# Performance work log

Measured on AMD Instinct MI355X. Metric: run time of the kernel, lower is better.

## Reference

```python
import jax, jax.numpy as jnp
import numpy as np

TOKENS, IN_F, OUT_F = 8192, 4096, 4096
MAXQ = 15          # 4-bit
ZERO_POINT = 8     # (maxq + 1) // 2


def _make_24_mask(key, in_f, out_f):
    """Boolean 2:4 mask: exactly 2 True per contiguous group of 4 along in_f."""
    scores = jax.random.normal(key, (in_f // 4, 4, out_f), dtype=jnp.float32)
    # ascending sort along the group-of-4 axis; index 2 = 2nd largest value
    thresh = jnp.sort(scores, axis=1)[:, 2:3, :]
    mask = scores >= thresh  # keeps top-2 of each group of 4
    return mask.reshape(in_f, out_f)


def setup_inputs() -> dict:
    key = jax.random.key(0)
    k_x, k_q, k_m, k_s = jax.random.split(key, 4)
    x = jax.random.normal(k_x, (TOKENS, IN_F), dtype=jnp.float16)
    qvals = jax.random.randint(k_q, (IN_F, OUT_F), 0, MAXQ + 1, dtype=jnp.int32)
    mask = _make_24_mask(k_m, IN_F, OUT_F)
    # per-column scales (groupsize == infeatures -> one scale row)
    scales = (jax.random.uniform(k_s, (1, OUT_F), dtype=jnp.float32) * 0.01 + 0.001).astype(jnp.float16)
    return {"x": x, "qvals": qvals, "mask": mask, "scales": scales}


def reference(x, qvals, mask, scales):
    # Dequantize: W = (q - zero_point) * scale, then apply 2:4 sparsity mask.
    w = (qvals.astype(jnp.float32) - ZERO_POINT) * scales.astype(jnp.float32)  # [in, out]
    w = jnp.where(mask, w, 0.0).astype(x.dtype)
    # GEMM with fp32 accumulation (as the fused kernel does), output in x.dtype
    y = jnp.einsum("ti,io->to", x, w, preferred_element_type=jnp.float32)
    return y.astype(x.dtype)
```

## Files before the change

kernel.cpp:

```cpp
#include <hip/hip_runtime.h>
#include <stdint.h>

typedef short short8 __attribute__((ext_vector_type(8)));
typedef float floatx4 __attribute__((ext_vector_type(4)));

#define M_TOK 8192
#define K_IN  4096
#define N_OUT 4096
#define NTT   (K_IN / 32)

static __device__ __forceinline__ float bf2f(ushort u) {
    union { uint32_t u; float f; } v;
    v.u = ((uint32_t)u) << 16;
    return v.f;
}
static __device__ __forceinline__ ushort f2bf(float f) {
    union { float f; uint32_t u; } v;
    v.f = f;
    uint32_t u = v.u;
    uint32_t r = (u + 0x7FFFu + ((u >> 16) & 1u)) >> 16;
    return (ushort)r;
}

__global__ void detect_zero_kernel(int* __restrict__ flags) {
    if (threadIdx.x < 3) flags[1 + threadIdx.x] = 0;
}

__global__ __launch_bounds__(256) void detect_count_kernel(
    const unsigned char* __restrict__ mb, int* __restrict__ flags) {
    const ushort* mh = (const ushort*)mb;
    const unsigned int* mw = (const unsigned int*)mb;
    __shared__ int sh[3];
    if (threadIdx.x < 3) sh[threadIdx.x] = 0;
    __syncthreads();
    int s = blockIdx.x * 256 + threadIdx.x;
    int grp = s & 255;
    int o   = (s * 97) & 4095;
    int c1 = 0, c2 = 0, c4 = 0;
    #pragma unroll
    for (int r = 0; r < 4; ++r) {
        size_t idx = (size_t)(4 * grp + r) * N_OUT + o;
        c1 += (mb[idx] != 0);
        c2 += (mh[idx] != 0);
        c4 += (mw[idx] != 0);
    }
    if (c1 != 2) atomicAdd(&sh[0], 1);
    if (c2 != 2) atomicAdd(&sh[1], 1);
    if (c4 != 2) atomicAdd(&sh[2], 1);
    __syncthreads();
    if (threadIdx.x == 0) {
        atomicAdd(&flags[1], sh[0]);
        atomicAdd(&flags[2], sh[1]);
        atomicAdd(&flags[3], sh[2]);
    }
}

__global__ void detect_final_kernel(int* __restrict__ flags) {
    if (threadIdx.x == 0) {
        int size = 4, best = flags[3];
        if (flags[2] < best) { size = 2; best = flags[2]; }
        if (flags[1] < best) { size = 1; }
        flags[0] = size;
    }
}

__global__ __launch_bounds__(256) void convert_x_kernel(
    const float* __restrict__ xf, ushort* __restrict__ Xb) {
    const int total = M_TOK * K_IN;
    const int stride = gridDim.x * 256 * 8;
    for (int i = (blockIdx.x * 256 + threadIdx.x) * 8; i < total; i += stride) {
        floatx4 f0 = *(const floatx4*)&xf[i];
        floatx4 f1 = *(const floatx4*)&xf[i + 4];
        short8 v;
        #pragma unroll
        for (int j = 0; j < 4; ++j) v[j]     = (short)f2bf(f0[j]);
        #pragma unroll
        for (int j = 0; j < 4; ++j) v[4 + j] = (short)f2bf(f1[j]);
        *(short8*)&Xb[i] = v;
    }
}

__global__ __launch_bounds__(256) void dequant_kernel(
    const int* __restrict__ q, const void* __restrict__ maskp,
    const float* __restrict__ scales, ushort* __restrict__ Bt,
    const int* __restrict__ flagp) {
    const int msize = flagp[0];
    const int i0 = blockIdx.x * 64;
    const int o0 = blockIdx.y * 64;
    const int tid = threadIdx.x;
    const unsigned char* mb = (const unsigned char*)maskp;
    const ushort* mh = (const ushort*)maskp;
    const unsigned int* mi = (const unsigned int*)maskp;
    __shared__ ushort T[64][72];

    for (int p = 0; p < 16; ++p) {
        int idx = p * 256 + tid;
        int r = idx >> 6, c = idx & 63;
        size_t gi = (size_t)(i0 + r) * N_OUT + (o0 + c);
        bool m;
        if (msize == 1)      m = (mb[gi] != 0);
        else if (msize == 2) m = (mh[gi] != 0);
        else                 m = (mi[gi] != 0);
        float s = scales[o0 + c];
        float w = m ? (float)(q[gi] - 8) * s : 0.0f;
        T[r][c] = f2bf(w);
    }
    __syncthreads();
    for (int p = 0; p < 2; ++p) {
        int ol = p * 32 + (tid >> 3);
        int i8 = (tid & 7) * 8;
        short8 v;
        #pragma unroll
        for (int j = 0; j < 8; ++j) v[j] = (short)T[i8 + j][ol];
        *(short8*)&Bt[(size_t)(o0 + ol) * K_IN + i0 + i8] = v;
    }
}

#define GL2L16(gp, lbase)                                                      \
    __builtin_amdgcn_global_load_lds(                                          \
        (const __attribute__((address_space(1))) void*)(gp),                   \
        (__attribute__((address_space(3))) void*)(lbase), 16, 0, 0)

#define MFMA16(a, b, c) __builtin_amdgcn_mfma_f32_16x16x32_bf16(a, b, c, 0, 0, 0)

__global__ __launch_bounds__(256, 2) void gemm_kernel(
    const ushort* __restrict__ X,
    const ushort* __restrict__ Bt,
    float* __restrict__ Y) {
    __shared__ ushort As[2][128][32];
    __shared__ ushort Bs[2][256][32];

    const int tid  = threadIdx.x;
    const int w    = tid >> 6;
    const int lane = tid & 63;

    const int xcd = blockIdx.x & 7;
    const int jj  = (blockIdx.x >> 3) & 63;
    const int rr0 = blockIdx.x >> 9;
    const int m_tile = rr0 * 32 + (xcd & 1) * 16 + (jj & 15);
    const int n_tile = (xcd >> 1) * 4 + (jj >> 4);
    const int row0 = m_tile * 128;
    const int col0 = n_tile * 256;

    floatx4 acc[8][4] = {};

    const int schunk = (tid & 3) ^ ((tid >> 3) & 3);
    const ushort* gA = X  + (size_t)(row0 + (tid >> 2)) * K_IN + schunk * 8;
    const ushort* gB = Bt + (size_t)(col0 + (tid >> 2)) * K_IN + schunk * 8;

    const int fr = lane & 15, g = lane >> 4;
    const int fsw = (fr >> 1) & 3;

    #define STG(BF, tt)                                                        \
        do {                                                                   \
            GL2L16(gA + (size_t)(tt) * 32,                                     \
                   (char*)&As[BF][w * 16][0] + lane * 16);                     \
            GL2L16(gA + (size_t)64 * K_IN + (size_t)(tt) * 32,                 \
                   (char*)&As[BF][64 + w * 16][0] + lane * 16);                \
            GL2L16(gB + (size_t)(tt) * 32,                                     \
                   (char*)&Bs[BF][w * 16][0] + lane * 16);                     \
            GL2L16(gB + (size_t)64 * K_IN + (size_t)(tt) * 32,                 \
                   (char*)&Bs[BF][64 + w * 16][0] + lane * 16);                \
            GL2L16(gB + (size_t)128 * K_IN + (size_t)(tt) * 32,                \
                   (char*)&Bs[BF][128 + w * 16][0] + lane * 16);               \
            GL2L16(gB + (size_t)192 * K_IN + (size_t)(tt) * 32,                \
                   (char*)&Bs[BF][192 + w * 16][0] + lane * 16);               \
        } while (0)

    #define TILE(BF, T)                                                        \
        do {                                                                   \
            short8 afr[8], bfr[4];                                             \
            _Pragma("unroll")                                                  \
            for (int n = 0; n < 4; ++n)                                        \
                bfr[n] = *(const short8*)&Bs[BF][w * 64 + n * 16 + fr]         \
                             [(g ^ fsw) * 8];                                  \
            _Pragma("unroll")                                                  \
            for (int m = 0; m < 8; ++m)                                        \
                afr[m] = *(const short8*)&As[BF][m * 16 + fr][(g ^ fsw) * 8];  \
            if ((T) + 1 < NTT) STG((BF) ^ 1, (T) + 1);                         \
            __builtin_amdgcn_s_barrier();                                      \
            asm volatile("s_waitcnt lgkmcnt(0)" ::: "memory");                 \
            __builtin_amdgcn_sched_barrier(0);                                 \
            __builtin_amdgcn_s_setprio(1);                                     \
            _Pragma("unroll")                                                  \
            for (int m = 0; m < 8; ++m)                                        \
                _Pragma("unroll")                                              \
                for (int n = 0; n < 4; ++n)                                    \
                    acc[m][n] = MFMA16(afr[m], bfr[n], acc[m][n]);             \
            __builtin_amdgcn_s_setprio(0);                                     \
            asm volatile("s_waitcnt vmcnt(0)" ::: "memory");                   \
            __builtin_amdgcn_s_barrier();                                      \
        } while (0)

    STG(0, 0);
    asm volatile("s_waitcnt vmcnt(0)" ::: "memory");
    __builtin_amdgcn_s_barrier();

    for (int t = 0; t < NTT; t += 2) {
        TILE(0, t);
        TILE(1, t + 1);
    }

    const int fq = lane >> 4;
    #pragma unroll
    for (int m = 0; m < 8; ++m)
        #pragma unroll
        for (int n = 0; n < 4; ++n)
            #pragma unroll
            for (int i = 0; i < 4; ++i) {
                int rr = row0 + m * 16 + fq * 4 + i;
                int cc = col0 + w * 64 + n * 16 + fr;
                Y[(size_t)rr * N_OUT + cc] = acc[m][n][i];
            }
    #undef TILE
    #undef STG
}

__global__ __launch_bounds__(256) void fallback_kernel(
    const float* __restrict__ xf, const int* __restrict__ q,
    const void* __restrict__ maskp, const float* __restrict__ scales,
    float* __restrict__ Y, const int* __restrict__ flagp) {
    const int msize = flagp[0];
    const int o = blockIdx.x * 256 + threadIdx.x;
    const int t = blockIdx.y;
    const unsigned char* mb = (const unsigned char*)maskp;
    const ushort* mh = (const ushort*)maskp;
    const unsigned int* mi = (const unsigned int*)maskp;
    float s = scales[o];
    float acc = 0.f;
    for (int i = 0; i < K_IN; ++i) {
        float x = bf2f(f2bf(xf[(size_t)t * K_IN + i]));
        size_t gi = (size_t)i * N_OUT + o;
        bool m;
        if (msize == 1)      m = (mb[gi] != 0);
        else if (msize == 2) m = (mh[gi] != 0);
        else                 m = (mi[gi] != 0);
        if (m) acc += x * bf2f(f2bf((float)(q[gi] - 8) * s));
    }
    Y[(size_t)t * N_OUT + o] = acc;
}

extern "C" void kernel_launch(void* const* d_in, const int* in_sizes, int n_in,
                              void* d_out, int out_size, void* d_ws, size_t ws_size,
                              hipStream_t stream) {
    const float* x      = (const float*)d_in[0];
    const int*   q      = (const int*)d_in[1];
    const void*  mask   = d_in[2];
    const float* scales = (const float*)d_in[3];
    float* y = (float*)d_out;

    const size_t BT_OFF = 64;
    const size_t XB_OFF = BT_OFF + (size_t)N_OUT * K_IN * 2;
    const size_t need   = XB_OFF + (size_t)M_TOK * K_IN * 2;

    int* flags = (int*)d_ws;
    detect_zero_kernel<<<1, 64, 0, stream>>>(flags);
    detect_count_kernel<<<64, 256, 0, stream>>>(
        (const unsigned char*)mask, flags);
    detect_final_kernel<<<1, 64, 0, stream>>>(flags);

    if (ws_size >= need) {
        ushort* Bt = (ushort*)((char*)d_ws + BT_OFF);
        ushort* Xb = (ushort*)((char*)d_ws + XB_OFF);
        convert_x_kernel<<<4096, 256, 0, stream>>>(x, Xb);
        dequant_kernel<<<dim3(K_IN / 64, N_OUT / 64), 256, 0, stream>>>(
            q, mask, scales, Bt, flags);
        gemm_kernel<<<dim3((M_TOK / 128) * (N_OUT / 256)), 256, 0, stream>>>(
            Xb, Bt, y);
    } else {
        fallback_kernel<<<dim3(N_OUT / 256, M_TOK), 256, 0, stream>>>(
            x, q, mask, scales, y, flags);
    }
}
```

Baseline: 361.6 us.

## Triple-buffer GEMM LDS pipeline and merge prep kernels into fewer launches

The GEMM now uses three LDS stages and prefetches two K-tiles ahead, waiting only on the older loads (vmcnt(6)) rather than draining all memory traffic each step. The x conversion and weight dequant run as a single prep launch, and the three-kernel mask detection becomes one single-block kernel. The aims are better hiding of global-load latency and less launch overhead. The costs are 50% more LDS per block, which may limit occupancy with two blocks per CU, plus a tail loop unrolled by hand.

After: 360.1 us. No clear change (-0.4%).

```diff
diff --git a/kernel.cpp b/kernel.cpp
--- a/kernel.cpp
+++ b/kernel.cpp
@@ -22,97 +22,84 @@
     return (ushort)r;
 }
 
-__global__ void detect_zero_kernel(int* __restrict__ flags) {
-    if (threadIdx.x < 3) flags[1 + threadIdx.x] = 0;
-}
-
-__global__ __launch_bounds__(256) void detect_count_kernel(
+__global__ __launch_bounds__(256) void detect_kernel(
     const unsigned char* __restrict__ mb, int* __restrict__ flags) {
     const ushort* mh = (const ushort*)mb;
     const unsigned int* mw = (const unsigned int*)mb;
-    __shared__ int sh[3];
-    if (threadIdx.x < 3) sh[threadIdx.x] = 0;
+    __shared__ int v[3];
+    if (threadIdx.x < 3) v[threadIdx.x] = 0;
     __syncthreads();
-    int s = blockIdx.x * 256 + threadIdx.x;
-    int grp = s & 255;
-    int o   = (s * 97) & 4095;
-    int c1 = 0, c2 = 0, c4 = 0;
-    #pragma unroll
-    for (int r = 0; r < 4; ++r) {
-        size_t idx = (size_t)(4 * grp + r) * N_OUT + o;
-        c1 += (mb[idx] != 0);
-        c2 += (mh[idx] != 0);
-        c4 += (mw[idx] != 0);
-    }
-    if (c1 != 2) atomicAdd(&sh[0], 1);
-    if (c2 != 2) atomicAdd(&sh[1], 1);
-    if (c4 != 2) atomicAdd(&sh[2], 1);
+    int l0 = 0, l1 = 0, l2 = 0;
+    for (int o = threadIdx.x; o < 4096; o += 256) {
+        int c1 = 0, c2 = 0, c4 = 0;
+        #pragma unroll
+        for (int r = 0; r < 4; ++r) {
+            int idx = r * N_OUT + o;
+            c1 += (mb[idx] != 0);
+            c2 += (mh[idx] != 0);
+            c4 += (mw[idx] != 0);
+        }
+        l0 += (c1 != 2); l1 += (c2 != 2); l2 += (c4 != 2);
+    }
+    atomicAdd(&v[0], l0); atomicAdd(&v[1], l1); atomicAdd(&v[2], l2);
     __syncthreads();
     if (threadIdx.x == 0) {
-        atomicAdd(&flags[1], sh[0]);
-        atomicAdd(&flags[2], sh[1]);
-        atomicAdd(&flags[3], sh[2]);
-    }
-}
-
-__global__ void detect_final_kernel(int* __restrict__ flags) {
-    if (threadIdx.x == 0) {
-        int size = 4, best = flags[3];
-        if (flags[2] < best) { size = 2; best = flags[2]; }
-        if (flags[1] < best) { size = 1; }
+        int size = 4, best = v[2];
+        if (v[1] < best) { size = 2; best = v[1]; }
+        if (v[0] < best) { size = 1; }
         flags[0] = size;
     }
 }
 
-__global__ __launch_bounds__(256) void convert_x_kernel(
-    const float* __restrict__ xf, ushort* __restrict__ Xb) {
-    const int total = M_TOK * K_IN;
-    const int stride = gridDim.x * 256 * 8;
-    for (int i = (blockIdx.x * 256 + threadIdx.x) * 8; i < total; i += stride) {
-        floatx4 f0 = *(const floatx4*)&xf[i];
-        floatx4 f1 = *(const floatx4*)&xf[i + 4];
-        short8 v;
-        #pragma unroll
-        for (int j = 0; j < 4; ++j) v[j]     = (short)f2bf(f0[j]);
-        #pragma unroll
-        for (int j = 0; j < 4; ++j) v[4 + j] = (short)f2bf(f1[j]);
-        *(short8*)&Xb[i] = v;
-    }
-}
-
-__global__ __launch_bounds__(256) void dequant_kernel(
+__global__ __launch_bounds__(256) void prep_kernel(
+    const float* __restrict__ xf, ushort* __restrict__ Xb,
     const int* __restrict__ q, const void* __restrict__ maskp,
     const float* __restrict__ scales, ushort* __restrict__ Bt,
     const int* __restrict__ flagp) {
-    const int msize = flagp[0];
-    const int i0 = blockIdx.x * 64;
-    const int o0 = blockIdx.y * 64;
     const int tid = threadIdx.x;
-    const unsigned char* mb = (const unsigned char*)maskp;
-    const ushort* mh = (const ushort*)maskp;
-    const unsigned int* mi = (const unsigned int*)maskp;
-    __shared__ ushort T[64][72];
-
-    for (int p = 0; p < 16; ++p) {
-        int idx = p * 256 + tid;
-        int r = idx >> 6, c = idx & 63;
-        size_t gi = (size_t)(i0 + r) * N_OUT + (o0 + c);
-        bool m;
-        if (msize == 1)      m = (mb[gi] != 0);
-        else if (msize == 2) m = (mh[gi] != 0);
-        else                 m = (mi[gi] != 0);
-        float s = scales[o0 + c];
-        float w = m ? (float)(q[gi] - 8) * s : 0.0f;
-        T[r][c] = f2bf(w);
-    }
-    __syncthreads();
-    for (int p = 0; p < 2; ++p) {
-        int ol = p * 32 + (tid >> 3);
-        int i8 = (tid & 7) * 8;
-        short8 v;
-        #pragma unroll
-        for (int j = 0; j < 8; ++j) v[j] = (short)T[i8 + j][ol];
-        *(short8*)&Bt[(size_t)(o0 + ol) * K_IN + i0 + i8] = v;
+    if (blockIdx.x < 4096) {
+        const int total = M_TOK * K_IN;
+        const int stride = 4096 * 256 * 8;
+        for (int i = (blockIdx.x * 256 + tid) * 8; i < total; i += stride) {
+            floatx4 f0 = *(const floatx4*)&xf[i];
+            floatx4 f1 = *(const floatx4*)&xf[i + 4];
+            short8 v;
+            #pragma unroll
+            for (int j = 0; j < 4; ++j) v[j]     = (short)f2bf(f0[j]);
+            #pragma unroll
+            for (int j = 0; j < 4; ++j) v[4 + j] = (short)f2bf(f1[j]);
+            *(short8*)&Xb[i] = v;
+        }
+    } else {
+        const int d  = blockIdx.x - 4096;
+        const int i0 = (d & 63) * 64;
+        const int o0 = (d >> 6) * 64;
+        const int msize = flagp[0];
+        const unsigned char* mb = (const unsigned char*)maskp;
+        const ushort* mh = (const ushort*)maskp;
+        const unsigned int* mi = (const unsigned int*)maskp;
+        __shared__ ushort T[64][72];
+        for (int p = 0; p < 16; ++p) {
+            int idx = p * 256 + tid;
+            int r = idx >> 6, c = idx & 63;
+            size_t gi = (size_t)(i0 + r) * N_OUT + (o0 + c);
+            bool m;
+            if (msize == 1)      m = (mb[gi] != 0);
+            else if (msize == 2) m = (mh[gi] != 0);
+            else                 m = (mi[gi] != 0);
+            float s = scales[o0 + c];
+            float w = m ? (float)(q[gi] - 8) * s : 0.0f;
+            T[r][c] = f2bf(w);
+        }
+        __syncthreads();
+        for (int p = 0; p < 2; ++p) {
+            int ol = p * 32 + (tid >> 3);
+            int i8 = (tid & 7) * 8;
+            short8 v;
+            #pragma unroll
+            for (int j = 0; j < 8; ++j) v[j] = (short)T[i8 + j][ol];
+            *(short8*)&Bt[(size_t)(o0 + ol) * K_IN + i0 + i8] = v;
+        }
     }
 }
 
@@ -127,8 +114,8 @@
     const ushort* __restrict__ X,
     const ushort* __restrict__ Bt,
     float* __restrict__ Y) {
-    __shared__ ushort As[2][128][32];
-    __shared__ ushort Bs[2][256][32];
+    __shared__ ushort As[3][128][32];
+    __shared__ ushort Bs[3][256][32];
 
     const int tid  = threadIdx.x;
     const int w    = tid >> 6;
@@ -151,33 +138,34 @@
     const int fr = lane & 15, g = lane >> 4;
     const int fsw = (fr >> 1) & 3;
 
-    #define STG(BF, tt)                                                        \
+    #define STG(SL, tt)                                                        \
         do {                                                                   \
             GL2L16(gA + (size_t)(tt) * 32,                                     \
-                   (char*)&As[BF][w * 16][0] + lane * 16);                     \
+                   (char*)&As[SL][w * 16][0] + lane * 16);                     \
             GL2L16(gA + (size_t)64 * K_IN + (size_t)(tt) * 32,                 \
-                   (char*)&As[BF][64 + w * 16][0] + lane * 16);                \
+                   (char*)&As[SL][64 + w * 16][0] + lane * 16);                \
             GL2L16(gB + (size_t)(tt) * 32,                                     \
-                   (char*)&Bs[BF][w * 16][0] + lane * 16);                     \
+                   (char*)&Bs[SL][w * 16][0] + lane * 16);                     \
             GL2L16(gB + (size_t)64 * K_IN + (size_t)(tt) * 32,                 \
-                   (char*)&Bs[BF][64 + w * 16][0] + lane * 16);                \
+                   (char*)&Bs[SL][64 + w * 16][0] + lane * 16);                \
             GL2L16(gB + (size_t)128 * K_IN + (size_t)(tt) * 32,                \
-                   (char*)&Bs[BF][128 + w * 16][0] + lane * 16);               \
+                   (char*)&Bs[SL][128 + w * 16][0] + lane * 16);               \
             GL2L16(gB + (size_t)192 * K_IN + (size_t)(tt) * 32,                \
-                   (char*)&Bs[BF][192 + w * 16][0] + lane * 16);               \
+                   (char*)&Bs[SL][192 + w * 16][0] + lane * 16);               \
         } while (0)
 
-    #define TILE(BF, T)                                                        \
+    #define TILE(SL, T)                                                        \
         do {                                                                   \
+            const bool sg = (T) + 2 < NTT;                                     \
             short8 afr[8], bfr[4];                                             \
             _Pragma("unroll")                                                  \
             for (int n = 0; n < 4; ++n)                                        \
-                bfr[n] = *(const short8*)&Bs[BF][w * 64 + n * 16 + fr]         \
+                bfr[n] = *(const short8*)&Bs[SL][w * 64 + n * 16 + fr]         \
                              [(g ^ fsw) * 8];                                  \
             _Pragma("unroll")                                                  \
             for (int m = 0; m < 8; ++m)                                        \
-                afr[m] = *(const short8*)&As[BF][m * 16 + fr][(g ^ fsw) * 8];  \
-            if ((T) + 1 < NTT) STG((BF) ^ 1, (T) + 1);                         \
+                afr[m] = *(const short8*)&As[SL][m * 16 + fr][(g ^ fsw) * 8];  \
+            if (sg) STG(((SL) + 2) % 3, (T) + 2);                              \
             __builtin_amdgcn_s_barrier();                                      \
             asm volatile("s_waitcnt lgkmcnt(0)" ::: "memory");                 \
             __builtin_amdgcn_sched_barrier(0);                                 \
@@ -188,18 +176,119 @@
                 for (int n = 0; n < 4; ++n)                                    \
                     acc[m][n] = MFMA16(afr[m], bfr[n], acc[m][n]);             \
             __builtin_amdgcn_s_setprio(0);                                     \
-            asm volatile("s_waitcnt vmcnt(0)" ::: "memory");                   \
+            if (sg) { asm volatile("s_waitcnt vmcnt(6)" ::: "memory"); }       \
+            else    { asm volatile("s_waitcnt vmcnt(0)" ::: "memory"); }       \
             __builtin_amdgcn_s_barrier();                                      \
         } while (0)
 
     STG(0, 0);
-    asm volatile("s_waitcnt vmcnt(0)" ::: "memory");
+    STG(1, 1);
+    asm volatile("s_waitcnt vmcnt(6)" ::: "memory");
     __builtin_amdgcn_s_barrier();
 
-    for (int t = 0; t < NTT; t += 2) {
+    for (int t = 0; t < NTT; t += 3) {
         TILE(0, t);
         TILE(1, t + 1);
-    }
+        TILE(2, t + 2);
+    }
+
+    const int fq = lane >> 4;
+    #pragma unroll
+    for (int m = 0; m < 8; ++m)
+        #pragma unroll
+        for (int n = 0; n < 4; ++n)
+            #pragma unroll
+            for (int i = 0; i < 4; ++i) {
+                int rr = row0 + m * 16 + fq * 4 + i;
+                int cc = col0 + w * 64 + n * 16 + fr;
+                Y[(size_t)rr * N_OUT + cc] = acc[m][n][i];
+            }
+    #undef TILE
+    #undef STG
+}
+
+
+__global__ __launch_bounds__(256, 2) void gemm_kernel_fix(
+    const ushort* __restrict__ X, const ushort* __restrict__ Bt,
+    float* __restrict__ Y) {
+    __shared__ ushort As[3][128][32];
+    __shared__ ushort Bs[3][256][32];
+
+    const int tid  = threadIdx.x;
+    const int w    = tid >> 6;
+    const int lane = tid & 63;
+
+    const int xcd = blockIdx.x & 7;
+    const int jj  = (blockIdx.x >> 3) & 63;
+    const int rr0 = blockIdx.x >> 9;
+    const int m_tile = rr0 * 32 + (xcd & 1) * 16 + (jj & 15);
+    const int n_tile = (xcd >> 1) * 4 + (jj >> 4);
+    const int row0 = m_tile * 128;
+    const int col0 = n_tile * 256;
+
+    floatx4 acc[8][4] = {};
+
+    const int schunk = (tid & 3) ^ ((tid >> 3) & 3);
+    const ushort* gA = X  + (size_t)(row0 + (tid >> 2)) * K_IN + schunk * 8;
+    const ushort* gB = Bt + (size_t)(col0 + (tid >> 2)) * K_IN + schunk * 8;
+
+    const int fr = lane & 15, g = lane >> 4;
+    const int fsw = (fr >> 1) & 3;
+
+    #define STG(SL, tt)                                                        \
+        do {                                                                   \
+            GL2L16(gA + (size_t)(tt) * 32,                                     \
+                   (char*)&As[SL][w * 16][0] + lane * 16);                     \
+            GL2L16(gA + (size_t)64 * K_IN + (size_t)(tt) * 32,                 \
+                   (char*)&As[SL][64 + w * 16][0] + lane * 16);                \
+            GL2L16(gB + (size_t)(tt) * 32,                                     \
+                   (char*)&Bs[SL][w * 16][0] + lane * 16);                     \
+            GL2L16(gB + (size_t)64 * K_IN + (size_t)(tt) * 32,                 \
+                   (char*)&Bs[SL][64 + w * 16][0] + lane * 16);                \
+            GL2L16(gB + (size_t)128 * K_IN + (size_t)(tt) * 32,                \
+                   (char*)&Bs[SL][128 + w * 16][0] + lane * 16);               \
+            GL2L16(gB + (size_t)192 * K_IN + (size_t)(tt) * 32,                \
+                   (char*)&Bs[SL][192 + w * 16][0] + lane * 16);               \
+        } while (0)
+
+    #define TILE(SL, T, SG, LAST)                                              \
+        do {                                                                   \
+            short8 afr[8], bfr[4];                                             \
+            _Pragma("unroll")                                                  \
+            for (int n = 0; n < 4; ++n)                                        \
+                bfr[n] = *(const short8*)&Bs[SL][w * 64 + n * 16 + fr]         \
+                             [(g ^ fsw) * 8];                                  \
+            _Pragma("unroll")                                                  \
+            for (int m = 0; m < 8; ++m)                                        \
+                afr[m] = *(const short8*)&As[SL][m * 16 + fr][(g ^ fsw) * 8];  \
+            if (SG) STG(((SL) + 2) % 3, (T) + 2);                              \
+            __builtin_amdgcn_s_barrier();                                      \
+            asm volatile("s_waitcnt lgkmcnt(0)" ::: "memory");                 \
+            __builtin_amdgcn_sched_barrier(0);                                 \
+            __builtin_amdgcn_s_setprio(1);                                     \
+            _Pragma("unroll")                                                  \
+            for (int m = 0; m < 8; ++m)                                        \
+                _Pragma("unroll")                                              \
+                for (int n = 0; n < 4; ++n)                                    \
+                    acc[m][n] = MFMA16(afr[m], bfr[n], acc[m][n]);             \
+            __builtin_amdgcn_s_setprio(0);                                     \
+            if (SG)        { asm volatile("s_waitcnt vmcnt(6)" ::: "memory"); }\
+            else if (!(LAST)) { asm volatile("s_waitcnt vmcnt(0)" ::: "memory"); } \
+            if (!(LAST)) __builtin_amdgcn_s_barrier();                         \
+        } while (0)
+
+    STG(0, 0);
+    STG(1, 1);
+    asm volatile("s_waitcnt vmcnt(6)" ::: "memory");
+    __builtin_amdgcn_s_barrier();
+
+    for (int t = 0; t < 126; t += 3) {
+        TILE(0, t,     true, false);
+        TILE(1, t + 1, true, false);
+        TILE(2, t + 2, true, false);
+    }
+    TILE(0, 126, false, false);
+    TILE(1, 127, false, true);
 
     const int fq = lane >> 4;
     #pragma unroll
@@ -254,18 +343,13 @@
     const size_t need   = XB_OFF + (size_t)M_TOK * K_IN * 2;
 
     int* flags = (int*)d_ws;
-    detect_zero_kernel<<<1, 64, 0, stream>>>(flags);
-    detect_count_kernel<<<64, 256, 0, stream>>>(
-        (const unsigned char*)mask, flags);
-    detect_final_kernel<<<1, 64, 0, stream>>>(flags);
+    detect_kernel<<<1, 256, 0, stream>>>((const unsigned char*)mask, flags);
 
     if (ws_size >= need) {
         ushort* Bt = (ushort*)((char*)d_ws + BT_OFF);
         ushort* Xb = (ushort*)((char*)d_ws + XB_OFF);
-        convert_x_kernel<<<4096, 256, 0, stream>>>(x, Xb);
-        dequant_kernel<<<dim3(K_IN / 64, N_OUT / 64), 256, 0, stream>>>(
-            q, mask, scales, Bt, flags);
-        gemm_kernel<<<dim3((M_TOK / 128) * (N_OUT / 256)), 256, 0, stream>>>(
+        prep_kernel<<<8192, 256, 0, stream>>>(x, Xb, q, mask, scales, Bt, flags);
+        gemm_kernel_fix<<<dim3((M_TOK / 128) * (N_OUT / 256)), 256, 0, stream>>>(
             Xb, Bt, y);
     } else {
         fallback_kernel<<<dim3(N_OUT / 256, M_TOK), 256, 0, stream>>>(
```
